# Performance work log

Measured on AMD Instinct MI355X. Metric: run time of the kernel, lower is better.

The kernel has to match this reference:

```python
import jax, jax.numpy as jnp
import numpy as np

B, S, H, L = 8, 4096, 768, 256   # batch, seq_len, hidden_size, num_lines (= line_ids.max()+1)
ATT_HID = 1024                    # attention MLP hidden dim from nn.Linear(hidden,1024)


def setup_inputs() -> dict:
    key = jax.random.key(0)
    k0, k1, k2, k3 = jax.random.split(key, 4)
    token_hidden = jax.random.normal(k0, (B, S, H), dtype=jnp.float32)
    line_ids = jax.random.randint(k1, (B, S), 0, L)  # all valid; -1 would mark invalid
    W1 = jax.random.normal(k2, (H, ATT_HID), dtype=jnp.float32) * 0.02
    b1 = jnp.zeros((ATT_HID,), jnp.float32)
    W2 = jax.random.normal(k3, (ATT_HID, 1), dtype=jnp.float32) * 0.02
    b2 = jnp.zeros((1,), jnp.float32)
    return {"token_hidden": token_hidden, "line_ids": line_ids,
            "W1": W1, "b1": b1, "W2": W2, "b2": b2}


def reference(token_hidden, line_ids, W1, b1, W2, b2):
    b, s, h = token_hidden.shape
    num_lines = L
    n_seg = b * num_lines + 1  # last segment is a dump slot for invalid (-1) tokens

    # attention scores: Linear -> tanh -> Linear, squeeze(-1)  [b, s]
    scores = (jnp.tanh(token_hidden @ W1 + b1) @ W2 + b2)[..., 0]

    valid = (line_ids >= 0).reshape(-1)                                   # [b*s]
    seg = jnp.where(line_ids >= 0,
                    jnp.arange(b)[:, None] * num_lines + line_ids,
                    b * num_lines).reshape(-1)                            # [b*s]
    s_flat = jnp.where(valid, scores.reshape(-1), -jnp.inf)

    # segment-wise stable softmax
    m = jax.ops.segment_max(s_flat, seg, num_segments=n_seg)
    m = jnp.where(jnp.isfinite(m), m, 0.0)  # empty segments -> safe 0
    e = jnp.where(valid, jnp.exp(scores.reshape(-1) - m[seg]), 0.0)
    denom = jax.ops.segment_sum(e, seg, num_segments=n_seg)
    w = e / jnp.maximum(denom[seg], 1e-20)                                # [b*s]

    # weighted sum of tokens per (batch, line) segment
    feats = jax.ops.segment_sum(token_hidden.reshape(-1, h) * w[:, None],
                                seg, num_segments=n_seg)
    line_features = feats[: b * num_lines].reshape(b, num_lines, h)

    counts = jax.ops.segment_sum(valid.astype(jnp.float32), seg, num_segments=n_seg)
    line_mask = counts[: b * num_lines].reshape(b, num_lines) > 0
    return line_features, line_mask
```

## Files before the change

### kernel.cpp

```cpp
#include <hip/hip_runtime.h>
#include <hip/hip_bf16.h>
#include <string.h>

#define M_TOK 32768
#define H_DIM 768
#define AH    1024
#define NSEG  2048
#define LCAP  192
#define CONV_BLOCKS 12288

typedef __attribute__((ext_vector_type(8))) __bf16 bf16x8;
typedef __attribute__((ext_vector_type(4))) float f32x4;

__device__ __forceinline__ float tanh_fast(float x) {
  float e = __expf(2.0f * x);
  return 1.0f - 2.0f * __builtin_amdgcn_rcpf(e + 1.0f);
}

__device__ __forceinline__ float bf2f(unsigned short u) {
  unsigned int v = (unsigned int)u << 16;
  float f;
  memcpy(&f, &v, 4);
  return f;
}

__global__ __launch_bounds__(256) void prep_kernel(
    const float* __restrict__ W1, __hip_bfloat16* __restrict__ W1t,
    const float4* __restrict__ X4, uint4* __restrict__ Xb4) {
  __shared__ float tile[32][33];
  if (blockIdx.x < 768) {
    int nt = blockIdx.x & 31, ktile = blockIdx.x >> 5;
    int n0 = nt * 32, k0 = ktile * 32;
    int tx = threadIdx.x & 31, ty = threadIdx.x >> 5;
    for (int r = ty; r < 32; r += 8)
      tile[r][tx] = W1[(size_t)(k0 + r) * AH + n0 + tx];
    __syncthreads();
    for (int r = ty; r < 32; r += 8)
      W1t[(size_t)(n0 + r) * H_DIM + k0 + tx] = __float2bfloat16(tile[tx][r]);
  } else {
    int i = (blockIdx.x - 768) * 256 + threadIdx.x;
    float4 v0 = X4[i * 2];
    float4 v1 = X4[i * 2 + 1];
    __hip_bfloat16 h[8] = {
        __float2bfloat16(v0.x), __float2bfloat16(v0.y),
        __float2bfloat16(v0.z), __float2bfloat16(v0.w),
        __float2bfloat16(v1.x), __float2bfloat16(v1.y),
        __float2bfloat16(v1.z), __float2bfloat16(v1.w)};
    uint4 p;
    memcpy(&p, h, 16);
    Xb4[i] = p;
  }
}

__global__ __launch_bounds__(256) void attn_score_kernel(
    const __hip_bfloat16* __restrict__ Xbg,
    const __hip_bfloat16* __restrict__ W1tg, const float* __restrict__ b1g,
    const float* __restrict__ W2g, float* __restrict__ scores2) {
  __shared__ __align__(16) __bf16 As[128 * 64];
  __shared__ __align__(16) __bf16 Bs[128 * 64];

  const int tid = threadIdx.x;
  const int bid = blockIdx.x;
  const int xcd = bid & 7;
  const int s   = bid >> 3;
  const int m0  = (xcd * 32 + (s >> 3)) * 128;
  const int nt  = s & 7;
  const int n0  = nt * 128;
  const int lane = tid & 63;
  const int wave = tid >> 6;
  const int wm   = (wave >> 1) * 64;
  const int wn   = (wave & 1) * 64;
  const int ml   = lane & 15;
  const int gsw  = lane & 7;

  const __bf16* Xb = (const __bf16*)Xbg;
  const __bf16* W  = (const __bf16*)W1tg;

  const int srow = tid >> 3;
  const int scol = ((tid & 7) ^ (srow & 7)) * 8;

  f32x4 acc[4][4];
#pragma unroll
  for (int i = 0; i < 4; i++)
#pragma unroll
    for (int j = 0; j < 4; j++) acc[i][j] = (f32x4)0.f;

  for (int kt = 0; kt < H_DIM; kt += 64) {
#pragma unroll
    for (int p = 0; p < 4; ++p) {
      const __bf16* ga = Xb + (size_t)(m0 + p * 32 + srow) * H_DIM + kt + scol;
      __builtin_amdgcn_global_load_lds(
          (const __attribute__((address_space(1))) void*)ga,
          (__attribute__((address_space(3))) void*)&As[p * 2048 + tid * 8],
          16, 0, 0);
      const __bf16* gb = W + (size_t)(n0 + p * 32 + srow) * H_DIM + kt + scol;
      __builtin_amdgcn_global_load_lds(
          (const __attribute__((address_space(1))) void*)gb,
          (__attribute__((address_space(3))) void*)&Bs[p * 2048 + tid * 8],
          16, 0, 0);
    }
    __syncthreads();

#pragma unroll
    for (int c = 0; c < 2; ++c) {
      const int gq = c * 4 + (lane >> 4);
      const int gp = (gq ^ gsw) * 8;
      bf16x8 af[4], bf[4];
#pragma unroll
      for (int i = 0; i < 4; i++)
        af[i] = *(const bf16x8*)&As[(wm + i * 16 + ml) * 64 + gp];
#pragma unroll
      for (int j = 0; j < 4; j++)
        bf[j] = *(const bf16x8*)&Bs[(wn + j * 16 + ml) * 64 + gp];

#pragma unroll
      for (int i = 0; i < 4; i++)
#pragma unroll
        for (int j = 0; j < 4; j++)
          acc[i][j] = __builtin_amdgcn_mfma_f32_16x16x32_bf16(af[i], bf[j],
                                                              acc[i][j], 0, 0, 0);
    }
    __syncthreads();
  }

  float b1v[4], w2v[4];
#pragma unroll
  for (int j = 0; j < 4; j++) {
    int n = n0 + wn + j * 16 + ml;
    b1v[j] = b1g[n];
    w2v[j] = W2g[n];
  }
  const int q4 = (lane >> 4) * 4;
  float tval[4][4];
#pragma unroll
  for (int i = 0; i < 4; i++) {
#pragma unroll
    for (int p = 0; p < 4; p++) {
      float t = 0.f;
#pragma unroll
      for (int j = 0; j < 4; j++)
        t += tanh_fast(acc[i][j][p] + b1v[j]) * w2v[j];
      t += __shfl_xor(t, 1);
      t += __shfl_xor(t, 2);
      t += __shfl_xor(t, 4);
      t += __shfl_xor(t, 8);
      tval[i][p] = t;
    }
  }
  float* redbuf = (float*)As;
  if ((wave & 1) && ml == 0) {
#pragma unroll
    for (int i = 0; i < 4; i++)
#pragma unroll
      for (int p = 0; p < 4; p++)
        redbuf[wm + i * 16 + q4 + p] = tval[i][p];
  }
  __syncthreads();
  if (!(wave & 1) && ml == 0) {
#pragma unroll
    for (int i = 0; i < 4; i++)
#pragma unroll
      for (int p = 0; p < 4; p++) {
        int row = wm + i * 16 + q4 + p;
        scores2[(size_t)(m0 + row) * 8 + nt] = tval[i][p] + redbuf[row];
      }
  }
}

__global__ __launch_bounds__(256) void aggregate_kernel(
    const ushort* __restrict__ Xb, const float* __restrict__ scores2,
    const int* __restrict__ line_ids, float4* __restrict__ out4,
    float* __restrict__ out_mask) {
  __shared__ int   slist[LCAP];
  __shared__ float sw[LCAP];
  __shared__ int   wvc[4];
  __shared__ float wred[4];
  const int seg = blockIdx.x;
  const int b = seg >> 8, lid = seg & 255;
  const int tid = threadIdx.x, lane = tid & 63, wave = tid >> 6;
  const int base = b * 4096;

  int ids[16];
#pragma unroll
  for (int c = 0; c < 16; ++c) ids[c] = line_ids[base + c * 256 + tid];

  int total = 0;
#pragma unroll
  for (int c = 0; c < 16; ++c) {
    bool match = (ids[c] == lid);
    unsigned long long mask = __ballot(match);
    if (lane == 0) wvc[wave] = __popcll(mask);
    __syncthreads();
    int off = total;
    for (int w = 0; w < wave; ++w) off += wvc[w];
    if (match) {
      int pos = off + __popcll(mask & ((1ull << lane) - 1ull));
      if (pos < LCAP) slist[pos] = base + c * 256 + tid;
    }
    total += wvc[0] + wvc[1] + wvc[2] + wvc[3];
    __syncthreads();
  }
  int cnt = total > LCAP ? LCAP : total;
  if (tid == 0) out_mask[seg] = cnt > 0 ? 1.f : 0.f;
  if (cnt == 0) {
    if (tid < H_DIM / 4)
      out4[(size_t)seg * (H_DIM / 4) + tid] = make_float4(0.f, 0.f, 0.f, 0.f);
    return;
  }
  float lmax = -3.4e38f;
  if (tid < cnt) {
    const float4* sp = (const float4*)(scores2 + (size_t)slist[tid] * 8);
    float4 a = sp[0], c4 = sp[1];
    float sc = ((a.x + a.y) + (a.z + a.w)) + ((c4.x + c4.y) + (c4.z + c4.w));
    sw[tid] = sc;
    lmax = sc;
  }
#pragma unroll
  for (int d = 1; d < 64; d <<= 1) lmax = fmaxf(lmax, __shfl_xor(lmax, d));
  if (lane == 0) wred[wave] = lmax;
  __syncthreads();
  float m = fmaxf(fmaxf(wred[0], wred[1]), fmaxf(wred[2], wred[3]));
  float lsum = 0.f;
  if (tid < cnt) {
    float e = __expf(sw[tid] - m);
    sw[tid] = e;
    lsum = e;
  }
#pragma unroll
  for (int d = 1; d < 64; d <<= 1) lsum += __shfl_xor(lsum, d);
  __syncthreads();
  if (lane == 0) wred[wave] = lsum;
  __syncthreads();
  float denom = wred[0] + wred[1] + wred[2] + wred[3];
  float inv = __builtin_amdgcn_rcpf(fmaxf(denom, 1e-20f));
  if (tid < cnt) sw[tid] *= inv;
  __syncthreads();
  if (tid < H_DIM / 4) {
    const ushort4* xb = (const ushort4*)Xb + tid;
    float4 acc = make_float4(0.f, 0.f, 0.f, 0.f);
    int t = 0;
    for (; t + 4 <= cnt; t += 4) {
      ushort4 u0 = xb[(size_t)slist[t]     * (H_DIM / 4)];
      ushort4 u1 = xb[(size_t)slist[t + 1] * (H_DIM / 4)];
      ushort4 u2 = xb[(size_t)slist[t + 2] * (H_DIM / 4)];
      ushort4 u3 = xb[(size_t)slist[t + 3] * (H_DIM / 4)];
      float w0 = sw[t], w1 = sw[t + 1], w2 = sw[t + 2], w3 = sw[t + 3];
      acc.x += w0 * bf2f(u0.x) + w1 * bf2f(u1.x) + w2 * bf2f(u2.x) + w3 * bf2f(u3.x);
      acc.y += w0 * bf2f(u0.y) + w1 * bf2f(u1.y) + w2 * bf2f(u2.y) + w3 * bf2f(u3.y);
      acc.z += w0 * bf2f(u0.z) + w1 * bf2f(u1.z) + w2 * bf2f(u2.z) + w3 * bf2f(u3.z);
      acc.w += w0 * bf2f(u0.w) + w1 * bf2f(u1.w) + w2 * bf2f(u2.w) + w3 * bf2f(u3.w);
    }
    for (; t < cnt; ++t) {
      ushort4 u = xb[(size_t)slist[t] * (H_DIM / 4)];
      float w = sw[t];
      acc.x += w * bf2f(u.x); acc.y += w * bf2f(u.y);
      acc.z += w * bf2f(u.z); acc.w += w * bf2f(u.w);
    }
    out4[(size_t)seg * (H_DIM / 4) + tid] = acc;
  }
}

extern "C" void kernel_launch(void* const* d_in, const int* in_sizes, int n_in,
                              void* d_out, int out_size, void* d_ws, size_t ws_size,
                              hipStream_t stream) {
  const float* X        = (const float*)d_in[0];
  const int*   line_ids = (const int*)d_in[1];
  const float* W1       = (const float*)d_in[2];
  const float* b1       = (const float*)d_in[3];
  const float* W2       = (const float*)d_in[4];

  char* p = (char*)d_ws;
  __hip_bfloat16* Xb      = (__hip_bfloat16*)p;  p += (size_t)M_TOK * H_DIM * 2;
  __hip_bfloat16* W1t     = (__hip_bfloat16*)p;  p += 1572864;
  float*          scores2 = (float*)p;           p += (size_t)M_TOK * 8 * 4;

  float* out_feats = (float*)d_out;
  float* out_mask  = out_feats + (size_t)NSEG * H_DIM;

  prep_kernel<<<768 + CONV_BLOCKS, 256, 0, stream>>>(
      W1, W1t, (const float4*)X, (uint4*)Xb);
  attn_score_kernel<<<2048, 256, 0, stream>>>(Xb, W1t, b1, W2, scores2);
  aggregate_kernel<<<NSEG, 256, 0, stream>>>((const ushort*)Xb, scores2,
                                             line_ids, (float4*)out_feats,
                                             out_mask);
}
```

Baseline: 247.7 us.

## Batch ballots in aggregate compaction, widen bf16 conversion with nontemporal loads

The aggregate kernel's token compaction now issues all 16 line_id loads and ballots up front, records per-chunk per-wave counts in shared memory, and computes positions after a single barrier, instead of two barriers per chunk. Score gathering is spread across 8 lanes per token with shuffle reductions, replacing one thread doing two float4 loads. The prep kernel converts 16 floats per thread using nontemporal loads and runs half as many conversion blocks. The aim is to cut barrier count and expose more memory-level parallelism, at the cost of more registers for the mask array and less thread-level parallelism in the conversion step.

```diff
diff --git a/kernel.cpp b/kernel.cpp
--- a/kernel.cpp
+++ b/kernel.cpp
@@ -7,7 +7,7 @@
 #define AH    1024
 #define NSEG  2048
 #define LCAP  192
-#define CONV_BLOCKS 12288
+#define CONV_BLOCKS 6144
 
 typedef __attribute__((ext_vector_type(8))) __bf16 bf16x8;
 typedef __attribute__((ext_vector_type(4))) float f32x4;
@@ -26,7 +26,7 @@
 
 __global__ __launch_bounds__(256) void prep_kernel(
     const float* __restrict__ W1, __hip_bfloat16* __restrict__ W1t,
-    const float4* __restrict__ X4, uint4* __restrict__ Xb4) {
+    const f32x4* __restrict__ X4, uint4* __restrict__ Xb4) {
   __shared__ float tile[32][33];
   if (blockIdx.x < 768) {
     int nt = blockIdx.x & 31, ktile = blockIdx.x >> 5;
@@ -38,17 +38,25 @@
     for (int r = ty; r < 32; r += 8)
       W1t[(size_t)(n0 + r) * H_DIM + k0 + tx] = __float2bfloat16(tile[tx][r]);
   } else {
-    int i = (blockIdx.x - 768) * 256 + threadIdx.x;
-    float4 v0 = X4[i * 2];
-    float4 v1 = X4[i * 2 + 1];
-    __hip_bfloat16 h[8] = {
-        __float2bfloat16(v0.x), __float2bfloat16(v0.y),
-        __float2bfloat16(v0.z), __float2bfloat16(v0.w),
-        __float2bfloat16(v1.x), __float2bfloat16(v1.y),
-        __float2bfloat16(v1.z), __float2bfloat16(v1.w)};
-    uint4 p;
-    memcpy(&p, h, 16);
-    Xb4[i] = p;
+    size_t i = (size_t)(blockIdx.x - 768) * 256 + threadIdx.x;
+    f32x4 v0 = __builtin_nontemporal_load(X4 + i * 4);
+    f32x4 v1 = __builtin_nontemporal_load(X4 + i * 4 + 1);
+    f32x4 v2 = __builtin_nontemporal_load(X4 + i * 4 + 2);
+    f32x4 v3 = __builtin_nontemporal_load(X4 + i * 4 + 3);
+    __hip_bfloat16 h[16] = {
+        __float2bfloat16(v0[0]), __float2bfloat16(v0[1]),
+        __float2bfloat16(v0[2]), __float2bfloat16(v0[3]),
+        __float2bfloat16(v1[0]), __float2bfloat16(v1[1]),
+        __float2bfloat16(v1[2]), __float2bfloat16(v1[3]),
+        __float2bfloat16(v2[0]), __float2bfloat16(v2[1]),
+        __float2bfloat16(v2[2]), __float2bfloat16(v2[3]),
+        __float2bfloat16(v3[0]), __float2bfloat16(v3[1]),
+        __float2bfloat16(v3[2]), __float2bfloat16(v3[3])};
+    uint4 p0, p1;
+    memcpy(&p0, h, 16);
+    memcpy(&p1, h + 8, 16);
+    Xb4[i * 2]     = p0;
+    Xb4[i * 2 + 1] = p1;
   }
 }
 
@@ -173,58 +181,63 @@
     float* __restrict__ out_mask) {
   __shared__ int   slist[LCAP];
   __shared__ float sw[LCAP];
-  __shared__ int   wvc[4];
+  __shared__ int   cw[16][4];
   __shared__ float wred[4];
   const int seg = blockIdx.x;
   const int b = seg >> 8, lid = seg & 255;
   const int tid = threadIdx.x, lane = tid & 63, wave = tid >> 6;
   const int base = b * 4096;
 
-  int ids[16];
-#pragma unroll
-  for (int c = 0; c < 16; ++c) ids[c] = line_ids[base + c * 256 + tid];
-
-  int total = 0;
+  unsigned long long mask[16];
 #pragma unroll
   for (int c = 0; c < 16; ++c) {
-    bool match = (ids[c] == lid);
-    unsigned long long mask = __ballot(match);
-    if (lane == 0) wvc[wave] = __popcll(mask);
-    __syncthreads();
-    int off = total;
-    for (int w = 0; w < wave; ++w) off += wvc[w];
-    if (match) {
-      int pos = off + __popcll(mask & ((1ull << lane) - 1ull));
+    int id = line_ids[base + c * 256 + tid];
+    mask[c] = __ballot(id == lid);
+    if (lane == 0) cw[c][wave] = __popcll(mask[c]);
+  }
+  __syncthreads();
+  const unsigned long long lmlt = (1ull << lane) - 1ull;
+  int run = 0;
+#pragma unroll
+  for (int c = 0; c < 16; ++c) {
+    if (mask[c] & (1ull << lane)) {
+      int o = run;
+      for (int w = 0; w < wave; ++w) o += cw[c][w];
+      int pos = o + __popcll(mask[c] & lmlt);
       if (pos < LCAP) slist[pos] = base + c * 256 + tid;
     }
-    total += wvc[0] + wvc[1] + wvc[2] + wvc[3];
-    __syncthreads();
-  }
-  int cnt = total > LCAP ? LCAP : total;
+    run += cw[c][0] + cw[c][1] + cw[c][2] + cw[c][3];
+  }
+  int cnt = run > LCAP ? LCAP : run;
   if (tid == 0) out_mask[seg] = cnt > 0 ? 1.f : 0.f;
+  __syncthreads();
   if (cnt == 0) {
     if (tid < H_DIM / 4)
       out4[(size_t)seg * (H_DIM / 4) + tid] = make_float4(0.f, 0.f, 0.f, 0.f);
     return;
   }
+  for (int t0 = 0; t0 < cnt; t0 += 32) {
+    int t = t0 + (tid >> 3);
+    float part = 0.f;
+    if (t < cnt) part = scores2[(size_t)slist[t] * 8 + (tid & 7)];
+    part += __shfl_xor(part, 1);
+    part += __shfl_xor(part, 2);
+    part += __shfl_xor(part, 4);
+    if (t < cnt && (tid & 7) == 0) sw[t] = part;
+  }
+  __syncthreads();
   float lmax = -3.4e38f;
-  if (tid < cnt) {
-    const float4* sp = (const float4*)(scores2 + (size_t)slist[tid] * 8);
-    float4 a = sp[0], c4 = sp[1];
-    float sc = ((a.x + a.y) + (a.z + a.w)) + ((c4.x + c4.y) + (c4.z + c4.w));
-    sw[tid] = sc;
-    lmax = sc;
-  }
+  if (tid < cnt) lmax = sw[tid];
 #pragma unroll
   for (int d = 1; d < 64; d <<= 1) lmax = fmaxf(lmax, __shfl_xor(lmax, d));
   if (lane == 0) wred[wave] = lmax;
   __syncthreads();
   float m = fmaxf(fmaxf(wred[0], wred[1]), fmaxf(wred[2], wred[3]));
   float lsum = 0.f;
+  float myexp = 0.f;
   if (tid < cnt) {
-    float e = __expf(sw[tid] - m);
-    sw[tid] = e;
-    lsum = e;
+    myexp = __expf(sw[tid] - m);
+    lsum = myexp;
   }
 #pragma unroll
   for (int d = 1; d < 64; d <<= 1) lsum += __shfl_xor(lsum, d);
@@ -233,7 +246,7 @@
   __syncthreads();
   float denom = wred[0] + wred[1] + wred[2] + wred[3];
   float inv = __builtin_amdgcn_rcpf(fmaxf(denom, 1e-20f));
-  if (tid < cnt) sw[tid] *= inv;
+  if (tid < cnt) sw[tid] = myexp * inv;
   __syncthreads();
   if (tid < H_DIM / 4) {
     const ushort4* xb = (const ushort4*)Xb + tid;
@@ -278,7 +291,7 @@
   float* out_mask  = out_feats + (size_t)NSEG * H_DIM;
 
   prep_kernel<<<768 + CONV_BLOCKS, 256, 0, stream>>>(
-      W1, W1t, (const float4*)X, (uint4*)Xb);
+      W1, W1t, (const f32x4*)X, (uint4*)Xb);
   attn_score_kernel<<<2048, 256, 0, stream>>>(Xb, W1t, b1, W2, scores2);
   aggregate_kernel<<<NSEG, 256, 0, stream>>>((const ushort*)Xb, scores2,
                                              line_ids, (float4*)out_feats,
```

Measured after the change: 257.0 us. 1.04x slower.
